# Kernel optimization log

Hardware: AMD Instinct MI355X
Metric: run time of the kernel (lower is better)

Reference implementation:

```python
import jax, jax.numpy as jnp
import numpy as np

N, C, H, L = 10000, 256, 8, 3
D = C // H  # per-head dim
E = 320000


def setup_inputs() -> dict:
    key = jax.random.key(0)
    ks = jax.random.split(key, 12)
    x = jax.random.normal(ks[0], (N, C), dtype=jnp.float32)
    edge_index = jax.random.randint(ks[1], (2, E), 0, N, dtype=jnp.int64)
    s = 0.02
    Wq = jax.random.normal(ks[2], (L, C, C), dtype=jnp.float32) * s
    Wk = jax.random.normal(ks[3], (L, C, C), dtype=jnp.float32) * s
    Wv = jax.random.normal(ks[4], (L, C, C), dtype=jnp.float32) * s
    Ws = jax.random.normal(ks[5], (L, C, C), dtype=jnp.float32) * s
    bq = jax.random.normal(ks[6], (L, C), dtype=jnp.float32) * s
    bk = jax.random.normal(ks[7], (L, C), dtype=jnp.float32) * s
    bv = jax.random.normal(ks[8], (L, C), dtype=jnp.float32) * s
    bs = jax.random.normal(ks[9], (L, C), dtype=jnp.float32) * s
    return {"x": x, "Wq": Wq, "bq": bq, "Wk": Wk, "bk": bk,
            "Wv": Wv, "bv": bv, "Ws": Ws, "bs": bs, "edge_index": edge_index}


def _transformer_conv(x, Wq, bq, Wk, bk, Wv, bv, Ws, bs, src, dst):
    # projections: [N, C] -> [N, H, D]
    q = (x @ Wq + bq).reshape(N, H, D)
    k = (x @ Wk + bk).reshape(N, H, D)
    v = (x @ Wv + bv).reshape(N, H, D)
    # per-edge attention scores: query at target, key/value at source
    score = jnp.einsum('ehd,ehd->eh', q[dst], k[src]) / jnp.sqrt(jnp.float32(D))  # [E, H]
    # scatter softmax over incoming edges per target node
    m = jax.ops.segment_max(score, dst, num_segments=N)            # [N, H]
    a = jnp.exp(score - m[dst])                                    # [E, H]
    denom = jax.ops.segment_sum(a, dst, num_segments=N)           # [N, H]
    alpha = a / (denom[dst] + 1e-16)                               # [E, H]
    # weighted aggregation of values
    msg = alpha[:, :, None] * v[src]                               # [E, H, D]
    out = jax.ops.segment_sum(msg, dst, num_segments=N).reshape(N, C)
    # root/skip connection
    return out + x @ Ws + bs


def reference(x, Wq, bq, Wk, bk, Wv, bv, Ws, bs, edge_index):
    src, dst = edge_index[0], edge_index[1]
    for l in range(L):
        x = _transformer_conv(x, Wq[l], bq[l], Wk[l], bk[l],
                              Wv[l], bv[l], Ws[l], bs[l], src, dst)
    return x
```

## Files before the change

kernel.cpp:

```cpp
#include <hip/hip_runtime.h>
#include <hip/hip_bf16.h>

#define N_NODES 10000
#define C_DIM   256
#define H_HEADS 8
#define D_HEAD  32
#define E_EDGES 320000
#define L_LAYERS 3
#define GN      1024

typedef __attribute__((ext_vector_type(8))) short bf16x8;
typedef __attribute__((ext_vector_type(4))) float f32x4;

__device__ __forceinline__ unsigned short f2b(float f) {
  __hip_bfloat16 h = __float2bfloat16(f);
  return *(unsigned short*)&h;
}

__device__ __forceinline__ float kv_lo(unsigned int w) {
  union { unsigned int u; float f; } c; c.u = w << 16; return c.f;
}
__device__ __forceinline__ float kv_hi(unsigned int w) {
  union { unsigned int u; float f; } c; c.u = w & 0xffff0000u; return c.f;
}

__device__ __forceinline__ float red8(float p) {
  p += __shfl_xor(p, 1);
  p += __shfl_xor(p, 2);
  p += __shfl_xor(p, 4);
  return p;
}

__device__ __forceinline__ float dot4(float4 q, uint4 w) {
  return fmaf(q.x, kv_lo(w.x),
         fmaf(q.y, kv_lo(w.y),
         fmaf(q.z, kv_lo(w.z), q.w * kv_lo(w.w))));
}

__device__ __forceinline__ void gload16(const void* g, void* l) {
  __builtin_amdgcn_global_load_lds(
      (const __attribute__((address_space(1))) unsigned int*)g,
      (__attribute__((address_space(3))) unsigned int*)l, 16, 0, 0);
}

__device__ __forceinline__ int colmap(int mat, int c) {
  if (mat == 0) return c;
  if (mat == 3) return 768 + c;
  return 256 + ((c >> 6) << 7) + ((mat - 1) << 6) + (c & 63);
}

__global__ void hist_kernel(const int* __restrict__ dst, int* __restrict__ deg) {
  int e = blockIdx.x * blockDim.x + threadIdx.x;
  if (e < E_EDGES) atomicAdd(&deg[dst[e]], 1);
}

__global__ __launch_bounds__(1024) void scan_kernel(const int* __restrict__ deg,
                                                    int* __restrict__ row_ptr) {
  __shared__ int part[1024];
  int t = threadIdx.x;
  const int CHUNK = (N_NODES + 1023) / 1024;
  int base = t * CHUNK;
  int s = 0;
  for (int i = 0; i < CHUNK; ++i) {
    int idx = base + i;
    if (idx < N_NODES) s += deg[idx];
  }
  part[t] = s;
  __syncthreads();
  for (int off = 1; off < 1024; off <<= 1) {
    int v = (t >= off) ? part[t - off] : 0;
    __syncthreads();
    part[t] += v;
    __syncthreads();
  }
  int run = (t == 0) ? 0 : part[t - 1];
  for (int i = 0; i < CHUNK; ++i) {
    int idx = base + i;
    if (idx <= N_NODES) {
      row_ptr[idx] = run;
      if (idx < N_NODES) run += deg[idx];
    }
  }
}

__global__ void scatter_kernel(const int* __restrict__ src, const int* __restrict__ dst,
                               const int* __restrict__ row_ptr, int* __restrict__ fill,
                               int* __restrict__ srcs) {
  int e = blockIdx.x * blockDim.x + threadIdx.x;
  if (e < E_EDGES) {
    int d = dst[e];
    int pos = atomicAdd(&fill[d], 1);
    srcs[row_ptr[d] + pos] = src[e];
  }
}

__global__ __launch_bounds__(256) void conv_all_kernel(
    const float* __restrict__ x, __hip_bfloat16* __restrict__ xb,
    const float* __restrict__ Wq, const float* __restrict__ Wk,
    const float* __restrict__ Wv, const float* __restrict__ Ws,
    __hip_bfloat16* __restrict__ Wt,
    const float* __restrict__ bq, const float* __restrict__ bk,
    const float* __restrict__ bv, const float* __restrict__ bs,
    float* __restrict__ biasf) {
  __shared__ float tt[32][33];
  int b = blockIdx.x, t = threadIdx.x;
  if (b < 2500) {
    int i = b * 256 + t;
    float4 f = *(const float4*)&x[(size_t)i * 4];
    union { unsigned short u[4]; uint2 w; } o;
    o.u[0] = f2b(f.x); o.u[1] = f2b(f.y); o.u[2] = f2b(f.z); o.u[3] = f2b(f.w);
    *(uint2*)&xb[(size_t)i * 4] = o.w;
  } else if (b < 3268) {
    int zz = b - 2500;
    int z = zz >> 6, tile = zz & 63;
    int l = z >> 2, mat = z & 3;
    const float* W = (mat == 0 ? Wq : mat == 1 ? Wk : mat == 2 ? Wv : Ws)
                     + (size_t)l * C_DIM * C_DIM;
    int k0 = (tile >> 3) * 32, c0 = (tile & 7) * 32;
    int tx = t & 31, ty = t >> 5;
    for (int i = 0; i < 32; i += 8)
      tt[ty + i][tx] = W[(k0 + ty + i) * C_DIM + c0 + tx];
    __syncthreads();
    for (int i = 0; i < 32; i += 8) {
      int ncol = colmap(mat, c0 + ty + i);
      Wt[(size_t)l * GN * C_DIM + (size_t)ncol * C_DIM + k0 + tx] =
          __float2bfloat16(tt[tx][ty + i]);
    }
  } else {
    int i = (b - 3268) * 256 + t;
    if (i < L_LAYERS * GN) {
      int l = i >> 10, n = i & 1023;
      int mat = n >> 8, c = n & 255;
      const float* bb = (mat == 0 ? bq : mat == 1 ? bk : mat == 2 ? bv : bs);
      biasf[l * GN + colmap(mat, c)] = bb[l * C_DIM + c];
    }
  }
}

__global__ __launch_bounds__(256) void gemm_kernel(
    const __hip_bfloat16* __restrict__ xb,
    const __hip_bfloat16* __restrict__ Wt,
    const float* __restrict__ biasf,
    float* __restrict__ q4,
    unsigned short* __restrict__ kvu,
    float* __restrict__ skip) {
  __shared__ __align__(16) unsigned short SH[16384];
  __hip_bfloat16* As = (__hip_bfloat16*)SH;
  __hip_bfloat16* Bs = (__hip_bfloat16*)(SH + 8192);
  int tid = threadIdx.x;
  int wid = tid >> 6, lane = tid & 63;
  int row0 = blockIdx.x * 128;
  int col0 = blockIdx.y * 128;
  int wr = wid >> 1, wc = wid & 1;
  int lr = lane & 15, lq = lane >> 4;
  int swz = (lr & 7) * 8;

  f32x4 acc[4][4] = {};

  for (int k0 = 0; k0 < C_DIM; k0 += 64) {
#pragma unroll
    for (int j = 0; j < 4; ++j) {
      int c = j * 256 + wid * 64 + lane;
      int arow = c >> 3;
      int kc = 8 * ((c & 7) ^ ((c >> 3) & 7));
      int grow = row0 + arow;
      if (grow > N_NODES - 1) grow = N_NODES - 1;
      gload16(xb + (size_t)grow * C_DIM + k0 + kc, As + (size_t)(j * 256 + wid * 64) * 8);
    }
#pragma unroll
    for (int j = 0; j < 4; ++j) {
      int c = j * 256 + wid * 64 + lane;
      int brow = c >> 3;
      int kc = 8 * ((c & 7) ^ ((c >> 3) & 7));
      gload16(Wt + (size_t)(col0 + brow) * C_DIM + k0 + kc,
              Bs + (size_t)(j * 256 + wid * 64) * 8);
    }
    __syncthreads();

#pragma unroll
    for (int ks = 0; ks < 2; ++ks) {
      bf16x8 fa[4], fb[4];
#pragma unroll
      for (int m = 0; m < 4; ++m)
        fa[m] = *(const bf16x8*)&As[(wr * 64 + m * 16 + lr) * 64 + ((ks * 32 + lq * 8) ^ swz)];
#pragma unroll
      for (int n = 0; n < 4; ++n)
        fb[n] = *(const bf16x8*)&Bs[(wc * 64 + n * 16 + lr) * 64 + ((ks * 32 + lq * 8) ^ swz)];
#pragma unroll
      for (int m = 0; m < 4; ++m)
#pragma unroll
        for (int n = 0; n < 4; ++n)
          acc[m][n] = __builtin_amdgcn_mfma_f32_16x16x32_bf16(fa[m], fb[n], acc[m][n], 0, 0, 0);
    }
    __syncthreads();
  }

  float bias_n[4];
#pragma unroll
  for (int n = 0; n < 4; ++n) bias_n[n] = biasf[col0 + wc * 64 + n * 16 + lr];

  if (col0 >= 256 && col0 < 768) {
    int half = wc;
#pragma unroll
    for (int m = 0; m < 4; ++m) {
#pragma unroll
      for (int n = 0; n < 4; ++n) {
        int chs = n * 16 + lr;
#pragma unroll
        for (int r = 0; r < 4; ++r) {
          int row = wr * 64 + m * 16 + lq * 4 + r;
          SH[row * 128 + chs * 2 + half] = f2b(acc[m][n][r] + bias_n[n]);
        }
      }
    }
    __syncthreads();
    int slice = (col0 - 256) >> 7;
    unsigned int* kvd = (unsigned int*)kvu;
    int t16 = tid & 15, rbase = tid >> 4;
#pragma unroll
    for (int it = 0; it < 8; ++it) {
      int row = it * 16 + rbase;
      int grow = row0 + row;
      if (grow < N_NODES) {
        uint4 vv = *(const uint4*)&SH[row * 128 + t16 * 8];
        *(uint4*)&kvd[((size_t)slice * N_NODES + grow) * 64 + t16 * 4] = vv;
      }
    }
  } else {
#pragma unroll
    for (int m = 0; m < 4; ++m) {
#pragma unroll
      for (int n = 0; n < 4; ++n) {
        int colG = col0 + wc * 64 + n * 16 + lr;
#pragma unroll
        for (int r = 0; r < 4; ++r) {
          int grow = row0 + wr * 64 + m * 16 + lq * 4 + r;
          if (grow < N_NODES) {
            float val = acc[m][n][r] + bias_n[n];
            if (col0 < 256) {
              q4[((size_t)(colG >> 6) * N_NODES + grow) * 64 + (colG & 63)] = val;
            } else {
              skip[(size_t)grow * C_DIM + (colG - 768)] = val;
            }
          }
        }
      }
    }
  }
}

__global__ __launch_bounds__(256) void agg_kernel(
    const float* __restrict__ q4,
    const unsigned int* __restrict__ kv4,
    const int* __restrict__ row_ptr, const int* __restrict__ srcs,
    float* __restrict__ out, __hip_bfloat16* __restrict__ xb_next) {
  int b = blockIdx.x;
  int u = b >> 3, r = b & 7;
  int slice = r >> 1;
  int wid = threadIdx.x >> 6, lane = threadIdx.x & 63;
  int n = ((((u << 1) | (r & 1)) << 2) + wid);
  int slot = lane >> 4;
  int l4 = (lane & 15) * 4;
  const size_t SB = (size_t)slice * N_NODES * 64;
  const float scl = 0.25503526f;

  float4 qv = *(const float4*)&q4[SB + (size_t)n * 64 + l4];
  qv.x *= scl; qv.y *= scl; qv.z *= scl; qv.w *= scl;
  const unsigned int* kvs = kv4 + SB;

  int beg = row_ptr[n], end = row_ptr[n + 1];
  float l = 0.f;
  float4 a = make_float4(0.f, 0.f, 0.f, 0.f);

  int i = beg;
  int sa1 = 0, sb1 = 0;
  uint4 wa = make_uint4(0, 0, 0, 0), wb = make_uint4(0, 0, 0, 0);
  if (i + 8 <= end) {
    int sa0 = srcs[i + slot], sb0 = srcs[i + 4 + slot];
    wa = *(const uint4*)&kvs[(size_t)sa0 * 64 + l4];
    wb = *(const uint4*)&kvs[(size_t)sb0 * 64 + l4];
    if (i + 16 <= end) { sa1 = srcs[i + 8 + slot]; sb1 = srcs[i + 12 + slot]; }
  }
  while (i + 8 <= end) {
    uint4 na = make_uint4(0, 0, 0, 0), nb = make_uint4(0, 0, 0, 0);
    if (i + 16 <= end) {
      na = *(const uint4*)&kvs[(size_t)sa1 * 64 + l4];
      nb = *(const uint4*)&kvs[(size_t)sb1 * 64 + l4];
      if (i + 24 <= end) {
        sa1 = srcs[i + 16 + slot]; sb1 = srcs[i + 20 + slot];
      }
    }
    float pa = red8(dot4(qv, wa));
    float pb = red8(dot4(qv, wb));
    float ea = exp2f(pa), eb = exp2f(pb);
    l += ea + eb;
    a.x = fmaf(ea, kv_hi(wa.x), fmaf(eb, kv_hi(wb.x), a.x));
    a.y = fmaf(ea, kv_hi(wa.y), fmaf(eb, kv_hi(wb.y), a.y));
    a.z = fmaf(ea, kv_hi(wa.z), fmaf(eb, kv_hi(wb.z), a.z));
    a.w = fmaf(ea, kv_hi(wa.w), fmaf(eb, kv_hi(wb.w), a.w));
    wa = na; wb = nb;
    i += 8;
  }
  for (; i < end; i += 4) {
    int j = i + slot;
    bool valid = j < end;
    int s = srcs[valid ? j : beg];
    uint4 w = *(const uint4*)&kvs[(size_t)s * 64 + l4];
    float p = red8(dot4(qv, w));
    float e = valid ? exp2f(p) : 0.f;
    l += e;
    a.x = fmaf(e, kv_hi(w.x), a.x);
    a.y = fmaf(e, kv_hi(w.y), a.y);
    a.z = fmaf(e, kv_hi(w.z), a.z);
    a.w = fmaf(e, kv_hi(w.w), a.w);
  }

#pragma unroll
  for (int mask = 16; mask <= 32; mask <<= 1) {
    l   += __shfl_xor(l, mask);
    a.x += __shfl_xor(a.x, mask);
    a.y += __shfl_xor(a.y, mask);
    a.z += __shfl_xor(a.z, mask);
    a.w += __shfl_xor(a.w, mask);
  }

  if (lane < 16) {
    float inv = 1.f / (l + 1e-16f);
    size_t idx = (size_t)n * C_DIM + slice * 64 + l4;
    float4 o = *(const float4*)&out[idx];
    o.x += a.x * inv; o.y += a.y * inv; o.z += a.z * inv; o.w += a.w * inv;
    *(float4*)&out[idx] = o;
    union { unsigned short us[4]; uint2 w; } ob;
    ob.us[0] = f2b(o.x); ob.us[1] = f2b(o.y); ob.us[2] = f2b(o.z); ob.us[3] = f2b(o.w);
    *(uint2*)&xb_next[idx] = ob.w;
  }
}

extern "C" void kernel_launch(void* const* d_in, const int* in_sizes, int n_in,
                              void* d_out, int out_size, void* d_ws, size_t ws_size,
                              hipStream_t stream) {
  const float* x0 = (const float*)d_in[0];
  const float* Wq = (const float*)d_in[1];
  const float* bq = (const float*)d_in[2];
  const float* Wk = (const float*)d_in[3];
  const float* bk = (const float*)d_in[4];
  const float* Wv = (const float*)d_in[5];
  const float* bv = (const float*)d_in[6];
  const float* Ws = (const float*)d_in[7];
  const float* bs = (const float*)d_in[8];
  const int* ei  = (const int*)d_in[9];
  const int* src = ei;
  const int* dst = ei + E_EDGES;
  float* out = (float*)d_out;

  const size_t NC = (size_t)N_NODES * C_DIM;
  __hip_bfloat16* xb = (__hip_bfloat16*)d_ws;
  unsigned int* kvbuf = (unsigned int*)(xb + NC);
  __hip_bfloat16* Wt = (__hip_bfloat16*)(kvbuf + NC);
  float* qbuf  = (float*)(Wt + (size_t)L_LAYERS * GN * C_DIM);
  float* skipA = qbuf + NC;
  float* biasf = skipA + NC;
  int* row_ptr = (int*)(biasf + L_LAYERS * GN);
  int* deg  = row_ptr + (N_NODES + 1);
  int* fill = deg + N_NODES;
  int* srcs = fill + N_NODES;

  hipMemsetAsync(deg, 0, 2 * N_NODES * sizeof(int), stream);
  hist_kernel<<<(E_EDGES + 255) / 256, 256, 0, stream>>>(dst, deg);
  scan_kernel<<<1, 1024, 0, stream>>>(deg, row_ptr);
  scatter_kernel<<<(E_EDGES + 255) / 256, 256, 0, stream>>>(src, dst, row_ptr, fill, srcs);

  conv_all_kernel<<<3281, 256, 0, stream>>>(x0, xb, Wq, Wk, Wv, Ws, Wt,
                                            bq, bk, bv, bs, biasf);

  for (int l = 0; l < L_LAYERS; ++l) {
    float* skip = (l == L_LAYERS - 1) ? out : skipA;
    gemm_kernel<<<dim3((N_NODES + 127) / 128, GN / 128), 256, 0, stream>>>(
        xb, Wt + (size_t)l * GN * C_DIM, biasf + l * GN, qbuf,
        (unsigned short*)kvbuf, skip);
    agg_kernel<<<dim3(N_NODES), 256, 0, stream>>>(
        qbuf, kvbuf, row_ptr, srcs, skip, xb);
  }
}
```

Before: 207.5 us.

## Split each node's edge list across two waves and use DPP reductions

The aggregation kernel now assigns two wavefronts per node-slice, each handling half of the incoming edges. The partial softmax sums and weighted accumulators are merged through shared memory behind a block barrier, and the grid size is doubled. The 8-lane dot-product reduction switches from shuffles to DPP row operations, and launch bounds request higher occupancy. This aims to raise parallelism and latency hiding in the gather-bound loop, at the cost of an extra LDS merge, a syncthreads, and more blocks.

```diff
diff --git a/kernel.cpp b/kernel.cpp
--- a/kernel.cpp
+++ b/kernel.cpp
@@ -24,10 +24,16 @@
   union { unsigned int u; float f; } c; c.u = w & 0xffff0000u; return c.f;
 }
 
+template <int CTRL>
+__device__ __forceinline__ float dpp_add(float v) {
+  union { int i; float f; } c;
+  c.i = __builtin_amdgcn_update_dpp(0, __builtin_bit_cast(int, v), CTRL, 0xf, 0xf, true);
+  return v + c.f;
+}
 __device__ __forceinline__ float red8(float p) {
-  p += __shfl_xor(p, 1);
-  p += __shfl_xor(p, 2);
-  p += __shfl_xor(p, 4);
+  p = dpp_add<0xB1>(p);
+  p = dpp_add<0x4E>(p);
+  p = dpp_add<0x141>(p);
   return p;
 }
 
@@ -249,16 +255,18 @@
   }
 }
 
-__global__ __launch_bounds__(256) void agg_kernel(
+__global__ __launch_bounds__(256, 8) void agg_kernel(
     const float* __restrict__ q4,
     const unsigned int* __restrict__ kv4,
     const int* __restrict__ row_ptr, const int* __restrict__ srcs,
     float* __restrict__ out, __hip_bfloat16* __restrict__ xb_next) {
+  __shared__ float MRG[4][16][5];
   int b = blockIdx.x;
   int u = b >> 3, r = b & 7;
   int slice = r >> 1;
   int wid = threadIdx.x >> 6, lane = threadIdx.x & 63;
-  int n = ((((u << 1) | (r & 1)) << 2) + wid);
+  int n = (((u << 1) | (r & 1)) << 1) + (wid >> 1);
+  int half = wid & 1;
   int slot = lane >> 4;
   int l4 = (lane & 15) * 4;
   const size_t SB = (size_t)slice * N_NODES * 64;
@@ -268,7 +276,14 @@
   qv.x *= scl; qv.y *= scl; qv.z *= scl; qv.w *= scl;
   const unsigned int* kvs = kv4 + SB;
 
-  int beg = row_ptr[n], end = row_ptr[n + 1];
+  int begN = row_ptr[n], endN = row_ptr[n + 1];
+  int cnt = endN - begN;
+  int hl = ((cnt >> 1) + 3) & ~3;
+  if (hl > cnt) hl = cnt;
+  int mid = begN + hl;
+  int beg = half ? mid : begN;
+  int end = half ? endN : mid;
+
   float l = 0.f;
   float4 a = make_float4(0.f, 0.f, 0.f, 0.f);
 
@@ -304,7 +319,7 @@
   for (; i < end; i += 4) {
     int j = i + slot;
     bool valid = j < end;
-    int s = srcs[valid ? j : beg];
+    int s = srcs[valid ? j : begN];
     uint4 w = *(const uint4*)&kvs[(size_t)s * 64 + l4];
     float p = red8(dot4(qv, w));
     float e = valid ? exp2f(p) : 0.f;
@@ -325,6 +340,16 @@
   }
 
   if (lane < 16) {
+    MRG[wid][lane][0] = l;
+    MRG[wid][lane][1] = a.x; MRG[wid][lane][2] = a.y;
+    MRG[wid][lane][3] = a.z; MRG[wid][lane][4] = a.w;
+  }
+  __syncthreads();
+  if (half == 0 && lane < 16) {
+    int pw = wid ^ 1;
+    l   += MRG[pw][lane][0];
+    a.x += MRG[pw][lane][1]; a.y += MRG[pw][lane][2];
+    a.z += MRG[pw][lane][3]; a.w += MRG[pw][lane][4];
     float inv = 1.f / (l + 1e-16f);
     size_t idx = (size_t)n * C_DIM + slice * 64 + l4;
     float4 o = *(const float4*)&out[idx];
@@ -365,7 +390,7 @@
   int* fill = deg + N_NODES;
   int* srcs = fill + N_NODES;
 
-  hipMemsetAsync(deg, 0, 2 * N_NODES * sizeof(int), stream);
+  (void)hipMemsetAsync(deg, 0, 2 * N_NODES * sizeof(int), stream);
   hist_kernel<<<(E_EDGES + 255) / 256, 256, 0, stream>>>(dst, deg);
   scan_kernel<<<1, 1024, 0, stream>>>(deg, row_ptr);
   scatter_kernel<<<(E_EDGES + 255) / 256, 256, 0, stream>>>(src, dst, row_ptr, fill, srcs);
@@ -378,7 +403,7 @@
     gemm_kernel<<<dim3((N_NODES + 127) / 128, GN / 128), 256, 0, stream>>>(
         xb, Wt + (size_t)l * GN * C_DIM, biasf + l * GN, qbuf,
         (unsigned short*)kvbuf, skip);
-    agg_kernel<<<dim3(N_NODES), 256, 0, stream>>>(
+    agg_kernel<<<dim3(2 * N_NODES), 256, 0, stream>>>(
         qbuf, kvbuf, row_ptr, srcs, skip, xb);
   }
 }
```

Result: slower. 222.7 us (+7.3%).

## Widen aggregation slices from four heads-pairs to two four-head slices

Applied to the files above, without the earlier changes.

Changes the q and packed k/v buffers from four 64-channel slices to two 128-channel slices. Each wavefront now covers 4 heads (32 lanes per edge, 2 edges in parallel) instead of 2 heads with 4 edges in parallel, which halves the aggregation grid and cuts per-edge index loads and recomputation across slices. Each gathered source row becomes a longer contiguous 512-byte read. The trade-off is less edge-level parallelism per wave and a longer serial loop per node.

```diff
diff --git a/kernel.cpp b/kernel.cpp
--- a/kernel.cpp
+++ b/kernel.cpp
@@ -141,7 +141,7 @@
     const __hip_bfloat16* __restrict__ xb,
     const __hip_bfloat16* __restrict__ Wt,
     const float* __restrict__ biasf,
-    float* __restrict__ q4,
+    float* __restrict__ q2,
     unsigned short* __restrict__ kvu,
     float* __restrict__ skip) {
   __shared__ __align__(16) unsigned short SH[16384];
@@ -214,7 +214,9 @@
       }
     }
     __syncthreads();
-    int slice = (col0 - 256) >> 7;
+    int bl = (col0 - 256) >> 7;
+    int sl = bl >> 1;
+    int h64 = (bl & 1) * 64;
     unsigned int* kvd = (unsigned int*)kvu;
     int t16 = tid & 15, rbase = tid >> 4;
 #pragma unroll
@@ -223,7 +225,7 @@
       int grow = row0 + row;
       if (grow < N_NODES) {
         uint4 vv = *(const uint4*)&SH[row * 128 + t16 * 8];
-        *(uint4*)&kvd[((size_t)slice * N_NODES + grow) * 64 + t16 * 4] = vv;
+        *(uint4*)&kvd[((size_t)sl * N_NODES + grow) * 128 + h64 + t16 * 4] = vv;
       }
     }
   } else {
@@ -238,7 +240,7 @@
           if (grow < N_NODES) {
             float val = acc[m][n][r] + bias_n[n];
             if (col0 < 256) {
-              q4[((size_t)(colG >> 6) * N_NODES + grow) * 64 + (colG & 63)] = val;
+              q2[((size_t)(colG >> 7) * N_NODES + grow) * 128 + (colG & 127)] = val;
             } else {
               skip[(size_t)grow * C_DIM + (colG - 768)] = val;
             }
@@ -250,23 +252,22 @@
 }
 
 __global__ __launch_bounds__(256) void agg_kernel(
-    const float* __restrict__ q4,
-    const unsigned int* __restrict__ kv4,
+    const float* __restrict__ q2,
+    const unsigned int* __restrict__ kv2,
     const int* __restrict__ row_ptr, const int* __restrict__ srcs,
     float* __restrict__ out, __hip_bfloat16* __restrict__ xb_next) {
   int b = blockIdx.x;
-  int u = b >> 3, r = b & 7;
-  int slice = r >> 1;
+  int slice = b & 1;
   int wid = threadIdx.x >> 6, lane = threadIdx.x & 63;
-  int n = ((((u << 1) | (r & 1)) << 2) + wid);
-  int slot = lane >> 4;
-  int l4 = (lane & 15) * 4;
-  const size_t SB = (size_t)slice * N_NODES * 64;
+  int n = (b >> 1) * 4 + wid;
+  int slot = lane >> 5;
+  int l4 = (lane & 31) * 4;
+  const size_t SB = (size_t)slice * N_NODES * 128;
   const float scl = 0.25503526f;
 
-  float4 qv = *(const float4*)&q4[SB + (size_t)n * 64 + l4];
+  float4 qv = *(const float4*)&q2[SB + (size_t)n * 128 + l4];
   qv.x *= scl; qv.y *= scl; qv.z *= scl; qv.w *= scl;
-  const unsigned int* kvs = kv4 + SB;
+  const unsigned int* kvs = kv2 + SB;
 
   int beg = row_ptr[n], end = row_ptr[n + 1];
   float l = 0.f;
@@ -275,19 +276,19 @@
   int i = beg;
   int sa1 = 0, sb1 = 0;
   uint4 wa = make_uint4(0, 0, 0, 0), wb = make_uint4(0, 0, 0, 0);
-  if (i + 8 <= end) {
-    int sa0 = srcs[i + slot], sb0 = srcs[i + 4 + slot];
-    wa = *(const uint4*)&kvs[(size_t)sa0 * 64 + l4];
-    wb = *(const uint4*)&kvs[(size_t)sb0 * 64 + l4];
-    if (i + 16 <= end) { sa1 = srcs[i + 8 + slot]; sb1 = srcs[i + 12 + slot]; }
-  }
-  while (i + 8 <= end) {
+  if (i + 4 <= end) {
+    int sa0 = srcs[i + slot], sb0 = srcs[i + 2 + slot];
+    wa = *(const uint4*)&kvs[(size_t)sa0 * 128 + l4];
+    wb = *(const uint4*)&kvs[(size_t)sb0 * 128 + l4];
+    if (i + 8 <= end) { sa1 = srcs[i + 4 + slot]; sb1 = srcs[i + 6 + slot]; }
+  }
+  while (i + 4 <= end) {
     uint4 na = make_uint4(0, 0, 0, 0), nb = make_uint4(0, 0, 0, 0);
-    if (i + 16 <= end) {
-      na = *(const uint4*)&kvs[(size_t)sa1 * 64 + l4];
-      nb = *(const uint4*)&kvs[(size_t)sb1 * 64 + l4];
-      if (i + 24 <= end) {
-        sa1 = srcs[i + 16 + slot]; sb1 = srcs[i + 20 + slot];
+    if (i + 8 <= end) {
+      na = *(const uint4*)&kvs[(size_t)sa1 * 128 + l4];
+      nb = *(const uint4*)&kvs[(size_t)sb1 * 128 + l4];
+      if (i + 12 <= end) {
+        sa1 = srcs[i + 8 + slot]; sb1 = srcs[i + 10 + slot];
       }
     }
     float pa = red8(dot4(qv, wa));
@@ -299,13 +300,13 @@
     a.z = fmaf(ea, kv_hi(wa.z), fmaf(eb, kv_hi(wb.z), a.z));
     a.w = fmaf(ea, kv_hi(wa.w), fmaf(eb, kv_hi(wb.w), a.w));
     wa = na; wb = nb;
-    i += 8;
-  }
-  for (; i < end; i += 4) {
+    i += 4;
+  }
+  for (; i < end; i += 2) {
     int j = i + slot;
     bool valid = j < end;
     int s = srcs[valid ? j : beg];
-    uint4 w = *(const uint4*)&kvs[(size_t)s * 64 + l4];
+    uint4 w = *(const uint4*)&kvs[(size_t)s * 128 + l4];
     float p = red8(dot4(qv, w));
     float e = valid ? exp2f(p) : 0.f;
     l += e;
@@ -315,18 +316,15 @@
     a.w = fmaf(e, kv_hi(w.w), a.w);
   }
 
-#pragma unroll
-  for (int mask = 16; mask <= 32; mask <<= 1) {
-    l   += __shfl_xor(l, mask);
-    a.x += __shfl_xor(a.x, mask);
-    a.y += __shfl_xor(a.y, mask);
-    a.z += __shfl_xor(a.z, mask);
-    a.w += __shfl_xor(a.w, mask);
-  }
-
-  if (lane < 16) {
+  l   += __shfl_xor(l, 32);
+  a.x += __shfl_xor(a.x, 32);
+  a.y += __shfl_xor(a.y, 32);
+  a.z += __shfl_xor(a.z, 32);
+  a.w += __shfl_xor(a.w, 32);
+
+  if (lane < 32) {
     float inv = 1.f / (l + 1e-16f);
-    size_t idx = (size_t)n * C_DIM + slice * 64 + l4;
+    size_t idx = (size_t)n * C_DIM + slice * 128 + l4;
     float4 o = *(const float4*)&out[idx];
     o.x += a.x * inv; o.y += a.y * inv; o.z += a.z * inv; o.w += a.w * inv;
     *(float4*)&out[idx] = o;
@@ -365,7 +363,7 @@
   int* fill = deg + N_NODES;
   int* srcs = fill + N_NODES;
 
-  hipMemsetAsync(deg, 0, 2 * N_NODES * sizeof(int), stream);
+  (void)hipMemsetAsync(deg, 0, 2 * N_NODES * sizeof(int), stream);
   hist_kernel<<<(E_EDGES + 255) / 256, 256, 0, stream>>>(dst, deg);
   scan_kernel<<<1, 1024, 0, stream>>>(deg, row_ptr);
   scatter_kernel<<<(E_EDGES + 255) / 256, 256, 0, stream>>>(src, dst, row_ptr, fill, srcs);
@@ -378,7 +376,7 @@
     gemm_kernel<<<dim3((N_NODES + 127) / 128, GN / 128), 256, 0, stream>>>(
         xb, Wt + (size_t)l * GN * C_DIM, biasf + l * GN, qbuf,
         (unsigned short*)kvbuf, skip);
-    agg_kernel<<<dim3(N_NODES), 256, 0, stream>>>(
+    agg_kernel<<<dim3(2 * (N_NODES / 4)), 256, 0, stream>>>(
         qbuf, kvbuf, row_ptr, srcs, skip, xb);
   }
 }
```

Result: faster. 201.5 us (median of 2 runs) (-2.9%).
